# Kernel optimization log

Measured on AMD Instinct MI355X. Metric: run time of the kernel, lower is better.

The kernel has to match this reference:

```python
import jax, jax.numpy as jnp
import numpy as np

B, L, D, W = 8, 512, 768, 12


def setup_inputs() -> dict:
    key = jax.random.key(0)
    k1, k2, k3, k4 = jax.random.split(key, 4)
    # kaiming_uniform-ish scale for conv weight: fan_in = D * W
    bound = float(np.sqrt(6.0 / (D * W)))
    return {
        "x": jax.random.normal(k1, (B, L, D), dtype=jnp.float32),
        "conv_w": jax.random.uniform(k2, (D, D, W), jnp.float32, -bound, bound),
        "proj_w": jax.random.normal(k3, (D, D), dtype=jnp.float32) * (1.0 / np.sqrt(D)),
        "proj_b": jax.random.normal(k4, (D,), dtype=jnp.float32) * 0.01,
    }


def reference(x, conv_w, proj_w, proj_b):
    # x: [B, L, D]; conv_w: [D_out, D_in, W]
    b, l, d = x.shape
    w = conv_w.shape[-1]
    # Right-pad sequence so every width-(i+1) conv produces exactly L outputs
    xpad = jnp.pad(x, ((0, 0), (0, w - 1), (0, 0)))  # [B, L+W-1, D]
    # Shifted views: xs[k, b, l, d] = xpad[b, l+k, d]  (small fixed loop over W taps)
    xs = jnp.stack([xpad[:, k:k + l, :] for k in range(w)], axis=0)  # [W, B, L, D]
    # Per-tap contribution: taps[k] = x_{l+k} @ conv_w[:, :, k]^T
    taps = jnp.einsum('kbld,odk->kblo', xs, conv_w)  # [W, B, L, D]
    # conv with kernel width i+1 == cumulative sum of the first i+1 taps
    spans = jnp.cumsum(taps, axis=0)                 # [W, B, L, D]
    spans = jnp.transpose(spans, (1, 2, 0, 3))       # [B, L, W, D]
    h = jax.nn.relu(spans)
    return jnp.einsum('blwd,od->blwo', h, proj_w) + proj_b
```

## Files before the change

### kernel.cpp

```cpp
#include <hip/hip_runtime.h>
#include <hip/hip_bf16.h>
#include <stdint.h>

#define L_SEQ   512
#define D_DIM   768
#define W_TAPS  12
#define LPAD    523
#define NROWS   4096
#define MROWS   49152
#define XPAD_ELEMS (8 * 523 * 768)
#define CWT_KSTRIDE (768 * 768)

typedef __attribute__((ext_vector_type(8))) short bf16x8;
typedef __attribute__((ext_vector_type(4))) float f32x4;

static __device__ __forceinline__ float bf2f(short s) {
    union { uint32_t u; float f; } c;
    c.u = ((uint32_t)(uint16_t)s) << 16;
    return c.f;
}
static __device__ __forceinline__ short f2bf(float f) {
    union { float f; uint32_t u; } c; c.f = f;
    uint32_t u = c.u + 0x7FFFu + ((c.u >> 16) & 1u);
    return (short)(u >> 16);
}

__global__ void pad_cast_x(const float* __restrict__ x, __hip_bfloat16* __restrict__ xpad) {
    int i = blockIdx.x * 256 + threadIdx.x;
    if (i >= XPAD_ELEMS / 4) return;
    int e = i * 4;
    int row = e / 768, col = e % 768;
    int b = row / 523, l = row % 523;
    short4 ov;
    if (l < L_SEQ) {
        const float4* src = (const float4*)&x[((size_t)(b * L_SEQ + l)) * 768 + col];
        float4 v = *src;
        ov.x = f2bf(v.x); ov.y = f2bf(v.y); ov.z = f2bf(v.z); ov.w = f2bf(v.w);
    } else {
        ov.x = 0; ov.y = 0; ov.z = 0; ov.w = 0;
    }
    *(short4*)&xpad[e] = ov;
}

__global__ void transpose_cw(const float* __restrict__ cw, __hip_bfloat16* __restrict__ cwt) {
    int blk = blockIdx.x;
    int c = blk / 12;
    int dc = (blk % 12) * 64;
    __shared__ float tile[768];
    int lane = threadIdx.x;
    const float* src = cw + (size_t)c * (768 * 12) + (size_t)dc * 12;
    #pragma unroll
    for (int j = 0; j < 12; ++j) tile[j * 64 + lane] = src[j * 64 + lane];
    __syncthreads();
    #pragma unroll
    for (int k = 0; k < 12; ++k) {
        cwt[(size_t)k * CWT_KSTRIDE + (size_t)c * 768 + dc + lane] =
            __float2bfloat16(tile[lane * 12 + k]);
    }
}

__global__ void cast_pw(const float* __restrict__ pw, __hip_bfloat16* __restrict__ pwb) {
    int i = blockIdx.x * 256 + threadIdx.x;
    int e = i * 4;
    float4 v = *(const float4*)&pw[e];
    short4 ov; ov.x = f2bf(v.x); ov.y = f2bf(v.y); ov.z = f2bf(v.z); ov.w = f2bf(v.w);
    *(short4*)&pwb[e] = ov;
}

__global__ __launch_bounds__(256, 2) void taps_gemm(
    const __hip_bfloat16* __restrict__ xpad,
    const __hip_bfloat16* __restrict__ cwt,
    __hip_bfloat16* __restrict__ taps)
{
    __shared__ __align__(16) __hip_bfloat16 At[128 * 64];
    __shared__ __align__(16) __hip_bfloat16 Bt[128 * 64];
    const int m0 = blockIdx.x * 128;
    const int n0 = blockIdx.y * 128;
    const int ktap = blockIdx.z;
    const int tid = threadIdx.x;
    const int lane = tid & 63;
    const int wv = tid >> 6;
    const int fr = lane & 15;
    const int fq = lane >> 4;
    const int wm = (wv >> 1) * 64;
    const int wn = (wv & 1) * 64;

    const __hip_bfloat16* asrc[4];
    const __hip_bfloat16* bsrc[4];
    int ldsoff[4];
    #pragma unroll
    for (int j = 0; j < 4; ++j) {
        int p = (wv * 4 + j) * 1024 + lane * 16;
        int row = p >> 7;
        int c16 = (p >> 4) & 7;
        ldsoff[j] = p >> 1;
        int gr = m0 + row;
        int b = gr >> 9, l = gr & 511;
        asrc[j] = xpad + ((size_t)(b * LPAD + l + ktap)) * 768 + c16 * 8;
        bsrc[j] = cwt + (size_t)ktap * CWT_KSTRIDE + (size_t)(n0 + row) * 768 + c16 * 8;
    }

    f32x4 acc[4][4];
    #pragma unroll
    for (int i = 0; i < 4; ++i)
        #pragma unroll
        for (int j = 0; j < 4; ++j)
            acc[i][j] = (f32x4){0.f, 0.f, 0.f, 0.f};

    for (int kt = 0; kt < 12; ++kt) {
        const int d0 = kt * 64;
        #pragma unroll
        for (int j = 0; j < 4; ++j) {
            __builtin_amdgcn_global_load_lds(
                (const __attribute__((address_space(1))) void*)(asrc[j] + d0),
                (__attribute__((address_space(3))) void*)(At + ldsoff[j]), 16, 0, 0);
            __builtin_amdgcn_global_load_lds(
                (const __attribute__((address_space(1))) void*)(bsrc[j] + d0),
                (__attribute__((address_space(3))) void*)(Bt + ldsoff[j]), 16, 0, 0);
        }
        __syncthreads();
        #pragma unroll
        for (int kk = 0; kk < 2; ++kk) {
            bf16x8 a[4], b[4];
            #pragma unroll
            for (int fm = 0; fm < 4; ++fm)
                a[fm] = *(const bf16x8*)&At[(wm + fm * 16 + fr) * 64 + kk * 32 + fq * 8];
            #pragma unroll
            for (int fn = 0; fn < 4; ++fn)
                b[fn] = *(const bf16x8*)&Bt[(wn + fn * 16 + fr) * 64 + kk * 32 + fq * 8];
            #pragma unroll
            for (int fm = 0; fm < 4; ++fm)
                #pragma unroll
                for (int fn = 0; fn < 4; ++fn)
                    acc[fm][fn] = __builtin_amdgcn_mfma_f32_16x16x32_bf16(
                        a[fm], b[fn], acc[fm][fn], 0, 0, 0);
        }
        __syncthreads();
    }

    #pragma unroll
    for (int fm = 0; fm < 4; ++fm) {
        int gr = m0 + wm + fm * 16 + fq * 4;
        #pragma unroll
        for (int fn = 0; fn < 4; ++fn) {
            int gc = n0 + wn + fn * 16 + fr;
            #pragma unroll
            for (int r = 0; r < 4; ++r) {
                taps[((size_t)(gr + r) * W_TAPS + ktap) * 768 + gc] =
                    __float2bfloat16(acc[fm][fn][r]);
            }
        }
    }
}

__global__ void cumsum_relu(__hip_bfloat16* __restrict__ taps) {
    int t = blockIdx.x * 256 + threadIdx.x;
    int r = t / 96;
    int c8 = (t % 96) * 8;
    __hip_bfloat16* p = taps + (size_t)r * (W_TAPS * 768) + c8;
    float run[8];
    #pragma unroll
    for (int j = 0; j < 8; ++j) run[j] = 0.f;
    for (int k = 0; k < 12; ++k) {
        bf16x8 v = *(bf16x8*)(p + (size_t)k * 768);
        bf16x8 o;
        #pragma unroll
        for (int j = 0; j < 8; ++j) {
            run[j] += bf2f(v[j]);
            o[j] = f2bf(fmaxf(run[j], 0.f));
        }
        *(bf16x8*)(p + (size_t)k * 768) = o;
    }
}

__global__ __launch_bounds__(256, 2) void proj_gemm(
    const __hip_bfloat16* __restrict__ h,
    const __hip_bfloat16* __restrict__ pw,
    const float* __restrict__ pb,
    float* __restrict__ out)
{
    __shared__ __align__(16) __hip_bfloat16 At[128 * 64];
    __shared__ __align__(16) __hip_bfloat16 Bt[128 * 64];
    const int m0 = blockIdx.x * 128;
    const int n0 = blockIdx.y * 128;
    const int tid = threadIdx.x;
    const int lane = tid & 63;
    const int wv = tid >> 6;
    const int fr = lane & 15;
    const int fq = lane >> 4;
    const int wm = (wv >> 1) * 64;
    const int wn = (wv & 1) * 64;

    const __hip_bfloat16* asrc[4];
    const __hip_bfloat16* bsrc[4];
    int ldsoff[4];
    #pragma unroll
    for (int j = 0; j < 4; ++j) {
        int p = (wv * 4 + j) * 1024 + lane * 16;
        int row = p >> 7;
        int c16 = (p >> 4) & 7;
        ldsoff[j] = p >> 1;
        asrc[j] = h + (size_t)(m0 + row) * 768 + c16 * 8;
        bsrc[j] = pw + (size_t)(n0 + row) * 768 + c16 * 8;
    }

    f32x4 acc[4][4];
    #pragma unroll
    for (int i = 0; i < 4; ++i)
        #pragma unroll
        for (int j = 0; j < 4; ++j)
            acc[i][j] = (f32x4){0.f, 0.f, 0.f, 0.f};

    for (int kt = 0; kt < 12; ++kt) {
        const int d0 = kt * 64;
        #pragma unroll
        for (int j = 0; j < 4; ++j) {
            __builtin_amdgcn_global_load_lds(
                (const __attribute__((address_space(1))) void*)(asrc[j] + d0),
                (__attribute__((address_space(3))) void*)(At + ldsoff[j]), 16, 0, 0);
            __builtin_amdgcn_global_load_lds(
                (const __attribute__((address_space(1))) void*)(bsrc[j] + d0),
                (__attribute__((address_space(3))) void*)(Bt + ldsoff[j]), 16, 0, 0);
        }
        __syncthreads();
        #pragma unroll
        for (int kk = 0; kk < 2; ++kk) {
            bf16x8 a[4], b[4];
            #pragma unroll
            for (int fm = 0; fm < 4; ++fm)
                a[fm] = *(const bf16x8*)&At[(wm + fm * 16 + fr) * 64 + kk * 32 + fq * 8];
            #pragma unroll
            for (int fn = 0; fn < 4; ++fn)
                b[fn] = *(const bf16x8*)&Bt[(wn + fn * 16 + fr) * 64 + kk * 32 + fq * 8];
            #pragma unroll
            for (int fm = 0; fm < 4; ++fm)
                #pragma unroll
                for (int fn = 0; fn < 4; ++fn)
                    acc[fm][fn] = __builtin_amdgcn_mfma_f32_16x16x32_bf16(
                        a[fm], b[fn], acc[fm][fn], 0, 0, 0);
        }
        __syncthreads();
    }

    #pragma unroll
    for (int fm = 0; fm < 4; ++fm) {
        int gr = m0 + wm + fm * 16 + fq * 4;
        #pragma unroll
        for (int fn = 0; fn < 4; ++fn) {
            int gc = n0 + wn + fn * 16 + fr;
            float bias = pb[gc];
            #pragma unroll
            for (int r = 0; r < 4; ++r) {
                out[(size_t)(gr + r) * 768 + gc] = acc[fm][fn][r] + bias;
            }
        }
    }
}

extern "C" void kernel_launch(void* const* d_in, const int* in_sizes, int n_in,
                              void* d_out, int out_size, void* d_ws, size_t ws_size,
                              hipStream_t stream) {
    const float* x  = (const float*)d_in[0];
    const float* cw = (const float*)d_in[1];
    const float* pw = (const float*)d_in[2];
    const float* pb = (const float*)d_in[3];
    float* out = (float*)d_out;
    char* ws = (char*)d_ws;

    __hip_bfloat16* xpad = (__hip_bfloat16*)(ws);
    __hip_bfloat16* cwt  = (__hip_bfloat16*)(ws + 6426624);
    __hip_bfloat16* pwb  = (__hip_bfloat16*)(ws + 20582400);
    __hip_bfloat16* taps = (__hip_bfloat16*)(ws + 21762048);
    if (ws_size < 97259520u) return;

    pad_cast_x <<<3138, 256, 0, stream>>>(x, xpad);
    transpose_cw<<<9216,  64, 0, stream>>>(cw, cwt);
    cast_pw    <<<576,  256, 0, stream>>>(pw, pwb);

    taps_gemm  <<<dim3(32, 6, 12), 256, 0, stream>>>(xpad, cwt, taps);
    cumsum_relu<<<1536, 256, 0, stream>>>(taps);
    proj_gemm  <<<dim3(384, 6),    256, 0, stream>>>(taps, pwb, pb, out);
}
```

Before: 363.1 us.

## Fuse cumsum and ReLU into conv GEMM by accumulating taps in registers

The taps GEMM now runs over all 12 taps inside one block, keeping the accumulator across taps. After each tap it stores relu(running sum) as the span output directly, which removes the separate cumsum_relu pass and its read-modify-write of the large taps buffer. Tile size shrinks to 64x96, giving 512 blocks instead of 2304, each with 12x more K work and less MFMA reuse per block. Both GEMMs also gain an XCD-aware block index remapping for L2 locality.

```diff
diff --git a/kernel.cpp b/kernel.cpp
--- a/kernel.cpp
+++ b/kernel.cpp
@@ -67,109 +67,98 @@
     *(short4*)&pwb[e] = ov;
 }
 
-__global__ __launch_bounds__(256, 2) void taps_gemm(
+__global__ __launch_bounds__(256, 2) void spans_gemm(
     const __hip_bfloat16* __restrict__ xpad,
     const __hip_bfloat16* __restrict__ cwt,
-    __hip_bfloat16* __restrict__ taps)
+    __hip_bfloat16* __restrict__ spans)
 {
-    __shared__ __align__(16) __hip_bfloat16 At[128 * 64];
-    __shared__ __align__(16) __hip_bfloat16 Bt[128 * 64];
-    const int m0 = blockIdx.x * 128;
-    const int n0 = blockIdx.y * 128;
-    const int ktap = blockIdx.z;
+    __shared__ __align__(16) __hip_bfloat16 At[64 * 64];
+    __shared__ __align__(16) __hip_bfloat16 Bt[96 * 64];
+    const int bid = blockIdx.x;
+    const int wid = (bid & 7) * 64 + (bid >> 3);
+    const int m0 = (wid >> 3) * 64;
+    const int n0 = (wid & 7) * 96;
     const int tid = threadIdx.x;
     const int lane = tid & 63;
-    const int wv = tid >> 6;
     const int fr = lane & 15;
     const int fq = lane >> 4;
-    const int wm = (wv >> 1) * 64;
-    const int wn = (wv & 1) * 64;
-
-    const __hip_bfloat16* asrc[4];
-    const __hip_bfloat16* bsrc[4];
-    int ldsoff[4];
-    #pragma unroll
-    for (int j = 0; j < 4; ++j) {
-        int p = (wv * 4 + j) * 1024 + lane * 16;
-        int row = p >> 7;
-        int c16 = (p >> 4) & 7;
-        ldsoff[j] = p >> 1;
+    const int wv = tid >> 6;
+    const int wm = (wv >> 1) * 32;
+    const int wn = (wv & 1) * 48;
+
+    const __hip_bfloat16* asrc[2]; int aoff[2];
+    const __hip_bfloat16* bsrc[3]; int boff[3];
+    #pragma unroll
+    for (int j = 0; j < 2; ++j) {
+        int chunk = tid + j * 256;
+        int row = chunk >> 3, c16 = chunk & 7;
+        aoff[j] = chunk * 8;
         int gr = m0 + row;
         int b = gr >> 9, l = gr & 511;
-        asrc[j] = xpad + ((size_t)(b * LPAD + l + ktap)) * 768 + c16 * 8;
-        bsrc[j] = cwt + (size_t)ktap * CWT_KSTRIDE + (size_t)(n0 + row) * 768 + c16 * 8;
-    }
-
-    f32x4 acc[4][4];
-    #pragma unroll
-    for (int i = 0; i < 4; ++i)
-        #pragma unroll
-        for (int j = 0; j < 4; ++j)
+        asrc[j] = xpad + (size_t)(b * LPAD + l) * 768 + c16 * 8;
+    }
+    #pragma unroll
+    for (int j = 0; j < 3; ++j) {
+        int chunk = tid + j * 256;
+        int row = chunk >> 3, c16 = chunk & 7;
+        boff[j] = chunk * 8;
+        bsrc[j] = cwt + (size_t)(n0 + row) * 768 + c16 * 8;
+    }
+
+    f32x4 acc[2][3];
+    #pragma unroll
+    for (int i = 0; i < 2; ++i)
+        #pragma unroll
+        for (int j = 0; j < 3; ++j)
             acc[i][j] = (f32x4){0.f, 0.f, 0.f, 0.f};
 
-    for (int kt = 0; kt < 12; ++kt) {
-        const int d0 = kt * 64;
-        #pragma unroll
-        for (int j = 0; j < 4; ++j) {
-            __builtin_amdgcn_global_load_lds(
-                (const __attribute__((address_space(1))) void*)(asrc[j] + d0),
-                (__attribute__((address_space(3))) void*)(At + ldsoff[j]), 16, 0, 0);
-            __builtin_amdgcn_global_load_lds(
-                (const __attribute__((address_space(1))) void*)(bsrc[j] + d0),
-                (__attribute__((address_space(3))) void*)(Bt + ldsoff[j]), 16, 0, 0);
-        }
-        __syncthreads();
-        #pragma unroll
-        for (int kk = 0; kk < 2; ++kk) {
-            bf16x8 a[4], b[4];
-            #pragma unroll
-            for (int fm = 0; fm < 4; ++fm)
-                a[fm] = *(const bf16x8*)&At[(wm + fm * 16 + fr) * 64 + kk * 32 + fq * 8];
-            #pragma unroll
-            for (int fn = 0; fn < 4; ++fn)
-                b[fn] = *(const bf16x8*)&Bt[(wn + fn * 16 + fr) * 64 + kk * 32 + fq * 8];
-            #pragma unroll
-            for (int fm = 0; fm < 4; ++fm)
-                #pragma unroll
-                for (int fn = 0; fn < 4; ++fn)
-                    acc[fm][fn] = __builtin_amdgcn_mfma_f32_16x16x32_bf16(
-                        a[fm], b[fn], acc[fm][fn], 0, 0, 0);
-        }
-        __syncthreads();
-    }
-
-    #pragma unroll
-    for (int fm = 0; fm < 4; ++fm) {
-        int gr = m0 + wm + fm * 16 + fq * 4;
-        #pragma unroll
-        for (int fn = 0; fn < 4; ++fn) {
-            int gc = n0 + wn + fn * 16 + fr;
-            #pragma unroll
-            for (int r = 0; r < 4; ++r) {
-                taps[((size_t)(gr + r) * W_TAPS + ktap) * 768 + gc] =
-                    __float2bfloat16(acc[fm][fn][r]);
+    for (int k = 0; k < 12; ++k) {
+        const size_t aofs = (size_t)k * 768;
+        const size_t bofs = (size_t)k * CWT_KSTRIDE;
+        for (int kt = 0; kt < 12; ++kt) {
+            const int d0 = kt * 64;
+            #pragma unroll
+            for (int j = 0; j < 2; ++j)
+                __builtin_amdgcn_global_load_lds(
+                    (const __attribute__((address_space(1))) void*)(asrc[j] + aofs + d0),
+                    (__attribute__((address_space(3))) void*)(At + aoff[j]), 16, 0, 0);
+            #pragma unroll
+            for (int j = 0; j < 3; ++j)
+                __builtin_amdgcn_global_load_lds(
+                    (const __attribute__((address_space(1))) void*)(bsrc[j] + bofs + d0),
+                    (__attribute__((address_space(3))) void*)(Bt + boff[j]), 16, 0, 0);
+            __syncthreads();
+            #pragma unroll
+            for (int kk = 0; kk < 2; ++kk) {
+                bf16x8 a[2], b[3];
+                #pragma unroll
+                for (int fm = 0; fm < 2; ++fm)
+                    a[fm] = *(const bf16x8*)&At[(wm + fm * 16 + fr) * 64 + kk * 32 + fq * 8];
+                #pragma unroll
+                for (int fn = 0; fn < 3; ++fn)
+                    b[fn] = *(const bf16x8*)&Bt[(wn + fn * 16 + fr) * 64 + kk * 32 + fq * 8];
+                #pragma unroll
+                for (int fm = 0; fm < 2; ++fm)
+                    #pragma unroll
+                    for (int fn = 0; fn < 3; ++fn)
+                        acc[fm][fn] = __builtin_amdgcn_mfma_f32_16x16x32_bf16(
+                            a[fm], b[fn], acc[fm][fn], 0, 0, 0);
             }
-        }
-    }
-}
-
-__global__ void cumsum_relu(__hip_bfloat16* __restrict__ taps) {
-    int t = blockIdx.x * 256 + threadIdx.x;
-    int r = t / 96;
-    int c8 = (t % 96) * 8;
-    __hip_bfloat16* p = taps + (size_t)r * (W_TAPS * 768) + c8;
-    float run[8];
-    #pragma unroll
-    for (int j = 0; j < 8; ++j) run[j] = 0.f;
-    for (int k = 0; k < 12; ++k) {
-        bf16x8 v = *(bf16x8*)(p + (size_t)k * 768);
-        bf16x8 o;
-        #pragma unroll
-        for (int j = 0; j < 8; ++j) {
-            run[j] += bf2f(v[j]);
-            o[j] = f2bf(fmaxf(run[j], 0.f));
-        }
-        *(bf16x8*)(p + (size_t)k * 768) = o;
+            __syncthreads();
+        }
+        #pragma unroll
+        for (int fm = 0; fm < 2; ++fm) {
+            int gr = m0 + wm + fm * 16 + fq * 4;
+            #pragma unroll
+            for (int fn = 0; fn < 3; ++fn) {
+                int gc = n0 + wn + fn * 16 + fr;
+                #pragma unroll
+                for (int r = 0; r < 4; ++r) {
+                    spans[((size_t)(gr + r) * W_TAPS + k) * 768 + gc] =
+                        __float2bfloat16(fmaxf(acc[fm][fn][r], 0.f));
+                }
+            }
+        }
     }
 }
 
@@ -181,8 +170,10 @@
 {
     __shared__ __align__(16) __hip_bfloat16 At[128 * 64];
     __shared__ __align__(16) __hip_bfloat16 Bt[128 * 64];
-    const int m0 = blockIdx.x * 128;
-    const int n0 = blockIdx.y * 128;
+    const int bid = blockIdx.x;
+    const int wid = (bid & 7) * 288 + (bid >> 3);
+    const int m0 = (wid / 6) * 128;
+    const int n0 = (wid % 6) * 128;
     const int tid = threadIdx.x;
     const int lane = tid & 63;
     const int wv = tid >> 6;
@@ -267,17 +258,16 @@
     float* out = (float*)d_out;
     char* ws = (char*)d_ws;
 
-    __hip_bfloat16* xpad = (__hip_bfloat16*)(ws);
-    __hip_bfloat16* cwt  = (__hip_bfloat16*)(ws + 6426624);
-    __hip_bfloat16* pwb  = (__hip_bfloat16*)(ws + 20582400);
-    __hip_bfloat16* taps = (__hip_bfloat16*)(ws + 21762048);
+    __hip_bfloat16* xpad  = (__hip_bfloat16*)(ws);
+    __hip_bfloat16* cwt   = (__hip_bfloat16*)(ws + 6426624);
+    __hip_bfloat16* pwb   = (__hip_bfloat16*)(ws + 20582400);
+    __hip_bfloat16* spans = (__hip_bfloat16*)(ws + 21762048);
     if (ws_size < 97259520u) return;
 
-    pad_cast_x <<<3138, 256, 0, stream>>>(x, xpad);
+    pad_cast_x  <<<3138, 256, 0, stream>>>(x, xpad);
     transpose_cw<<<9216,  64, 0, stream>>>(cw, cwt);
-    cast_pw    <<<576,  256, 0, stream>>>(pw, pwb);
-
-    taps_gemm  <<<dim3(32, 6, 12), 256, 0, stream>>>(xpad, cwt, taps);
-    cumsum_relu<<<1536, 256, 0, stream>>>(taps);
-    proj_gemm  <<<dim3(384, 6),    256, 0, stream>>>(taps, pwb, pb, out);
-}
+    cast_pw     <<<576,  256, 0, stream>>>(pw, pwb);
+
+    spans_gemm  <<<512,  256, 0, stream>>>(xpad, cwt, spans);
+    proj_gemm   <<<2304, 256, 0, stream>>>(spans, pwb, pb, out);
+}
```

After: 387.9 us. +6.8%, slower.
